# Optimization experiments

Hardware: AMD Instinct MI355X
Metric: run time of the kernel (lower is better)

Reference implementation:

```python
import jax, jax.numpy as jnp
import numpy as np

A = -0.75  # PyTorch bicubic coefficient (a=-0.75)


def _cubic_taps(n):
    # output coord i maps to src = i/2 - 0.25 (align_corners=False, scale=2)
    i = np.arange(2 * n)
    src = i / 2.0 - 0.25
    base = np.floor(src).astype(np.int64)
    t = src - base
    offs = np.array([-1, 0, 1, 2])
    idx = np.clip(base[:, None] + offs[None, :], 0, n - 1)  # (2n,4) replicate border
    d = np.abs(t[:, None] - offs[None, :])
    w = np.where(d <= 1.0,
                 (A + 2) * d ** 3 - (A + 3) * d ** 2 + 1.0,
                 A * d ** 3 - 5 * A * d ** 2 + 8 * A * d - 4 * A)
    return jnp.asarray(idx), jnp.asarray(w.astype(np.float32))


def _upsample2_bicubic(x):
    B, C, H, W = x.shape
    ih, wh = _cubic_taps(H)
    iw, ww = _cubic_taps(W)
    x = (x[:, :, ih, :] * wh[None, None, :, :, None]).sum(3)   # (B,C,2H,W)
    x = (x[:, :, :, iw] * ww[None, None, None, :, :]).sum(4)   # (B,C,2H,2W)
    return x


def _conv2d(x, w, b, pad):
    y = jax.lax.conv_general_dilated(x, w, (1, 1), ((pad, pad), (pad, pad)),
                                     dimension_numbers=('NCHW', 'OIHW', 'NCHW'))
    return y + b[None, :, None, None]


def _instance_norm(x, w, b, eps=1e-5):
    m = x.mean(axis=(2, 3), keepdims=True)
    v = x.var(axis=(2, 3), keepdims=True)
    return (x - m) * jax.lax.rsqrt(v + eps) * w[None, :, None, None] + b[None, :, None, None]


def _prelu(x, a):
    return jnp.where(x >= 0, x, a * x)


def _unfold5(x):
    # 5x5 neighborhoods, pad=2 -> (B, C, 25, H, W); row-major kernel tap order
    B, C, H, W = x.shape
    xp = jnp.pad(x, ((0, 0), (0, 0), (2, 2), (2, 2)))
    return jnp.stack([xp[:, :, i:i + H, j:j + W] for i in range(5) for j in range(5)], axis=2)


def _forward(input, feature, conv1_w, conv1_b, in1_w, in1_b, prelu1_a,
             conv2_w, conv2_b, in2_w, in2_b, prelu2_a,
             res_w, res_b, feat_w, feat_b, pac_w, pac_b):
    # main mapping: conv-IN-PReLU x2
    y = _prelu(_instance_norm(_conv2d(input, conv1_w, conv1_b, 1), in1_w, in1_b), prelu1_a)
    y = _prelu(_instance_norm(_conv2d(y, conv2_w, conv2_b, 1), in2_w, in2_b), prelu2_a)
    # residual 1x1 mapping (in_channels != out_channels)
    y = y + _conv2d(input, res_w, res_b, 0)
    y = _upsample2_bicubic(y)                               # (B,O,2H,2W)
    # PAC guidance: gaussian kernel from 1x1-mapped feature, normalized over window
    g = _conv2d(feature, feat_w, feat_b, 0)                 # (B,O,2H,2W)
    gcols = _unfold5(g)                                     # (B,O,25,2H,2W)
    diff2 = ((gcols - g[:, :, None]) ** 2).sum(axis=1)      # (B,25,2H,2W)
    kern = jnp.exp(-0.5 * diff2)
    kern = kern / kern.sum(axis=1, keepdims=True)           # normalize_kernel=True
    xcols = _unfold5(y)                                     # (B,O,25,2H,2W)
    O, Ci = pac_w.shape[0], pac_w.shape[1]
    out = jnp.einsum('ocp,bcphw,bphw->bohw', pac_w.reshape(O, Ci, 25), xcols, kern)
    return out + pac_b[None, :, None, None]


def setup_inputs() -> dict:
    key = jax.random.key(0)
    ks = jax.random.split(key, 8)
    Cin, Cout, Cf = 256, 128, 128
    B, H, W = 2, 48, 48
    f32 = jnp.float32

    def w(k, shape, fan_in):
        return jax.random.normal(k, shape, f32) / np.float32(np.sqrt(fan_in))

    return {
        'input': jax.random.normal(ks[0], (B, Cin, H, W), f32),
        'feature': jax.random.normal(ks[1], (B, Cf, 2 * H, 2 * W), f32),
        'conv1_w': w(ks[2], (Cout, Cin, 3, 3), Cin * 9), 'conv1_b': jnp.zeros((Cout,), f32),
        'in1_w': jnp.ones((Cout,), f32), 'in1_b': jnp.zeros((Cout,), f32),
        'prelu1_a': jnp.asarray(0.25, f32),
        'conv2_w': w(ks[3], (Cout, Cout, 3, 3), Cout * 9), 'conv2_b': jnp.zeros((Cout,), f32),
        'in2_w': jnp.ones((Cout,), f32), 'in2_b': jnp.zeros((Cout,), f32),
        'prelu2_a': jnp.asarray(0.25, f32),
        'res_w': w(ks[4], (Cout, Cin, 1, 1), Cin), 'res_b': jnp.zeros((Cout,), f32),
        'feat_w': w(ks[5], (Cout, Cf, 1, 1), Cf), 'feat_b': jnp.zeros((Cout,), f32),
        'pac_w': w(ks[6], (Cout, Cout, 5, 5), Cout * 25), 'pac_b': jnp.zeros((Cout,), f32),
    }


def reference(input, feature, conv1_w, conv1_b, in1_w, in1_b, prelu1_a,
              conv2_w, conv2_b, in2_w, in2_b, prelu2_a,
              res_w, res_b, feat_w, feat_b, pac_w, pac_b):
    return _forward(input, feature, conv1_w, conv1_b, in1_w, in1_b, prelu1_a,
                    conv2_w, conv2_b, in2_w, in2_b, prelu2_a,
                    res_w, res_b, feat_w, feat_b, pac_w, pac_b)
```

## Files before the change

kernel.cpp:

```cpp
#include <hip/hip_runtime.h>
#include <hip/hip_bf16.h>

typedef __attribute__((ext_vector_type(8))) short bf16x8;
typedef __attribute__((ext_vector_type(4))) float f32x4;

constexpr int B   = 2;
constexpr int CIN = 256;
constexpr int CO  = 128;
constexpr int H = 48, W = 48;
constexpr int H2 = 96, W2 = 96;
constexpr int NPIX1 = H * W;
constexpr int NPIX2 = H2 * W2;
constexpr int NS = 4;

__device__ inline ushort f2bf(float v)
{
  __hip_bfloat16 h = __float2bfloat16(v);
  return *reinterpret_cast<ushort*>(&h);
}

__global__ __launch_bounds__(256) void prep_weights_kernel(
    const float* __restrict__ pac_w, const float* __restrict__ conv1_w,
    const float* __restrict__ conv2_w, const float* __restrict__ feat_w,
    const float* __restrict__ res_w,
    ushort* __restrict__ wbb, ushort* __restrict__ wt1, ushort* __restrict__ wt2,
    ushort* __restrict__ fwb, ushort* __restrict__ wrb)
{
  int blk = blockIdx.x, tid = threadIdx.x;
  if (blk < 1600) {
    int idx = blk * 256 + tid;
    int c = idx & 127, o = (idx >> 7) & 127, p = idx >> 14;
    wbb[idx] = f2bf(pac_w[((size_t)o * CO + c) * 25 + p]);
  } else if (blk < 2752) {
    int idx = (blk - 1600) * 256 + tid;
    int ci = idx & 255, o = (idx >> 8) & 127, tap = idx >> 15;
    wt1[idx] = f2bf(conv1_w[((size_t)o * CIN + ci) * 9 + tap]);
  } else if (blk < 3328) {
    int idx = (blk - 2752) * 256 + tid;
    int ci = idx & 127, o = (idx >> 7) & 127, tap = idx >> 14;
    wt2[idx] = f2bf(conv2_w[((size_t)o * CO + ci) * 9 + tap]);
  } else if (blk < 3392) {
    int idx = (blk - 3328) * 256 + tid;
    fwb[idx] = f2bf(feat_w[idx]);
  } else {
    int idx = (blk - 3392) * 256 + tid;
    wrb[idx] = f2bf(res_w[idx]);
  }
}

__global__ __launch_bounds__(256) void cvt_both_kernel(
    const float* __restrict__ input, const float* __restrict__ feature,
    ushort* __restrict__ xinh, ushort* __restrict__ fh)
{
  __shared__ float lt[32][65];
  int tid = threadIdx.x;
  if (blockIdx.x < 576) {
    int blk = blockIdx.x;
    int cg = blk & 7;
    int pc = (blk >> 3) % 36;
    int b  = blk / (8 * 36);
    int c0 = cg * 32, pix0 = pc * 64;
#pragma unroll
    for (int r = 0; r < 8; r++) {
      int c_l = r * 4 + (tid >> 6), px = tid & 63;
      lt[c_l][px] = input[((size_t)b * CIN + c0 + c_l) * NPIX1 + pix0 + px];
    }
    __syncthreads();
    int c_l = tid & 31;
#pragma unroll
    for (int r = 0; r < 8; r++) {
      int px = r * 8 + (tid >> 5);
      xinh[((size_t)b * NPIX1 + pix0 + px) * CIN + c0 + c_l] = f2bf(lt[c_l][px]);
    }
  } else {
    int blk = blockIdx.x - 576;
    int cg = blk & 3;
    int pc = (blk >> 2) % 144;
    int b  = blk / (4 * 144);
    int c0 = cg * 32, pix0 = pc * 64;
#pragma unroll
    for (int r = 0; r < 8; r++) {
      int c_l = r * 4 + (tid >> 6), px = tid & 63;
      lt[c_l][px] = feature[((size_t)b * CO + c0 + c_l) * NPIX2 + pix0 + px];
    }
    __syncthreads();
    int c_l = tid & 31;
#pragma unroll
    for (int r = 0; r < 8; r++) {
      int px = r * 8 + (tid >> 5);
      fh[((size_t)b * NPIX2 + pix0 + px) * CO + c0 + c_l] = f2bf(lt[c_l][px]);
    }
  }
}

template<int CIg>
__device__ __forceinline__ void conv3_body(
    int blk, int tid, char* smraw,
    const ushort* __restrict__ xh, const ushort* __restrict__ wt,
    float* __restrict__ pout)
{
  constexpr int CS = CIg / NS;
  constexpr int G  = CS / 8;
  constexpr int KC = CS / 32;
  ushort* xt = (ushort*)smraw;
  int tile = blk % 36;
  int s = (blk / 36) & 3;
  int b = blk / 144;
  int th = tile / 3, tw = tile % 3;
  int h0 = th * 4, w0 = tw * 16;
  int lane = tid & 63, wv = tid >> 6;
  int l15 = lane & 15, l4 = (lane >> 4) & 3;

  for (int q = tid; q < 108 * G; q += 256) {
    int pixi = q / G, g = q & (G - 1);
    int rh = pixi / 18, rw = pixi - rh * 18;
    int hg = h0 - 1 + rh, wg = w0 - 1 + rw;
    uint4 v{0u, 0u, 0u, 0u};
    if (hg >= 0 && hg < H && wg >= 0 && wg < W)
      v = *(const uint4*)(xh + (size_t)(b * NPIX1 + hg * W + wg) * CIg + s * CS + g * 8);
    *(uint4*)(xt + pixi * CS + ((g ^ (pixi & (G - 1))) * 8)) = v;
  }
  __syncthreads();

  int wo = wv * 32;
  const ushort* wbase = wt + (size_t)(wo + l15) * CIg + s * CS + l4 * 8;

  f32x4 acc0[4], acc1[4];
#pragma unroll
  for (int nf = 0; nf < 4; nf++) {
    acc0[nf] = {0.f, 0.f, 0.f, 0.f};
    acc1[nf] = {0.f, 0.f, 0.f, 0.f};
  }

  bf16x8 aC0[KC], aC1[KC], aN0[KC], aN1[KC];
#pragma unroll
  for (int kc = 0; kc < KC; kc++) {
    aC0[kc] = *(const bf16x8*)(wbase + kc * 32);
    aC1[kc] = *(const bf16x8*)(wbase + 16 * CIg + kc * 32);
  }

#pragma unroll 1
  for (int tap = 0; tap < 9; ++tap) {
    if (tap < 8) {
      const ushort* wn = wbase + (size_t)(tap + 1) * 128 * CIg;
#pragma unroll
      for (int kc = 0; kc < KC; kc++) {
        aN0[kc] = *(const bf16x8*)(wn + kc * 32);
        aN1[kc] = *(const bf16x8*)(wn + 16 * CIg + kc * 32);
      }
    }
    int kh = (tap >= 6) ? 2 : ((tap >= 3) ? 1 : 0);
    int kw = tap - kh * 3;
#pragma unroll
    for (int kc = 0; kc < KC; kc++) {
#pragma unroll
      for (int nf = 0; nf < 4; nf++) {
        int pix = (nf + kh) * 18 + kw + l15;
        bf16x8 bb = *(const bf16x8*)(xt + pix * CS + (((kc * 4 + l4) ^ (pix & (G - 1))) * 8));
        acc0[nf] = __builtin_amdgcn_mfma_f32_16x16x32_bf16(aC0[kc], bb, acc0[nf], 0, 0, 0);
        acc1[nf] = __builtin_amdgcn_mfma_f32_16x16x32_bf16(aC1[kc], bb, acc1[nf], 0, 0, 0);
      }
    }
#pragma unroll
    for (int kc = 0; kc < KC; kc++) { aC0[kc] = aN0[kc]; aC1[kc] = aN1[kc]; }
  }

#pragma unroll
  for (int nf = 0; nf < 4; nf++) {
    int pixg = (h0 + nf) * W + w0 + l15;
#pragma unroll
    for (int r = 0; r < 4; r++) {
      int o = wo + l4 * 4 + r;
      pout[((size_t)(s * B + b) * CO + o) * NPIX1 + pixg] = acc0[nf][r];
      pout[((size_t)(s * B + b) * CO + o + 16) * NPIX1 + pixg] = acc1[nf][r];
    }
  }
}

__device__ __forceinline__ void gemm_res_body(
    int blk, int tid, char* smraw,
    const ushort* __restrict__ xh, const ushort* __restrict__ wrb,
    const float* __restrict__ bias, float* __restrict__ out)
{
  ushort* xt = (ushort*)smraw;
  int pc = blk % 72;
  int b  = blk / 72;
  int pix0 = pc * 32;
  int lane = tid & 63, wv = tid >> 6;
  int l15 = lane & 15, l4 = (lane >> 4) & 3;

  for (int q = tid; q < 1024; q += 256) {
    int pixi = q >> 5, g = q & 31;
    uint4 v = *(const uint4*)(xh + (((size_t)b * NPIX1 + pix0 + pixi) << 8) + (g << 3));
    *(uint4*)(xt + (pixi << 8) + ((g ^ (pixi & 31)) << 3)) = v;
  }
  __syncthreads();

  int wo = wv * 32;
  const ushort* wbase = wrb + (size_t)(wo + l15) * CIN + l4 * 8;
  bf16x8 a0[8], a1[8];
#pragma unroll
  for (int kc = 0; kc < 8; kc++) {
    a0[kc] = *(const bf16x8*)(wbase + kc * 32);
    a1[kc] = *(const bf16x8*)(wbase + 16 * CIN + kc * 32);
  }
  f32x4 acc0[2], acc1[2];
#pragma unroll
  for (int nf = 0; nf < 2; nf++) {
    acc0[nf] = {0.f, 0.f, 0.f, 0.f};
    acc1[nf] = {0.f, 0.f, 0.f, 0.f};
  }
#pragma unroll
  for (int nf = 0; nf < 2; nf++) {
    int pix = nf * 16 + l15;
    int base = pix << 8;
    int sw = pix & 31;
#pragma unroll
    for (int kc = 0; kc < 8; kc++) {
      bf16x8 bb = *(const bf16x8*)(xt + base + ((((kc << 2) + l4) ^ sw) << 3));
      acc0[nf] = __builtin_amdgcn_mfma_f32_16x16x32_bf16(a0[kc], bb, acc0[nf], 0, 0, 0);
      acc1[nf] = __builtin_amdgcn_mfma_f32_16x16x32_bf16(a1[kc], bb, acc1[nf], 0, 0, 0);
    }
  }
#pragma unroll
  for (int nf = 0; nf < 2; nf++) {
    int gp = pix0 + nf * 16 + l15;
#pragma unroll
    for (int r = 0; r < 4; r++) {
      int o = wo + l4 * 4 + r;
      out[((size_t)b * CO + o) * NPIX1 + gp] = acc0[nf][r] + bias[o];
      out[((size_t)b * CO + o + 16) * NPIX1 + gp] = acc1[nf][r] + bias[o + 16];
    }
  }
}

__device__ __forceinline__ void gemm1x1_body(
    int blk, int tid, char* smraw,
    const ushort* __restrict__ fh, const ushort* __restrict__ fwb,
    const float* __restrict__ bias, float* __restrict__ out)
{
  ushort* xt = (ushort*)smraw;
  int pc = blk % 144;
  int b  = blk / 144;
  int pix0 = pc * 64;
  int lane = tid & 63, wv = tid >> 6;
  int l15 = lane & 15, l4 = (lane >> 4) & 3;

  for (int q = tid; q < 1024; q += 256) {
    int pixi = q >> 4, g = q & 15;
    uint4 v = *(const uint4*)(fh + (((size_t)b * NPIX2 + pix0 + pixi) << 7) + (g << 3));
    *(uint4*)(xt + (pixi << 7) + ((g ^ (pixi & 15)) << 3)) = v;
  }
  __syncthreads();

  int wo = wv * 32;
  const ushort* wbase = fwb + (size_t)(wo + l15) * CO + l4 * 8;
  bf16x8 a0[4], a1[4];
#pragma unroll
  for (int kc = 0; kc < 4; kc++) {
    a0[kc] = *(const bf16x8*)(wbase + kc * 32);
    a1[kc] = *(const bf16x8*)(wbase + 16 * CO + kc * 32);
  }
  f32x4 acc0[4], acc1[4];
#pragma unroll
  for (int nf = 0; nf < 4; nf++) {
    acc0[nf] = {0.f, 0.f, 0.f, 0.f};
    acc1[nf] = {0.f, 0.f, 0.f, 0.f};
  }
#pragma unroll
  for (int nf = 0; nf < 4; nf++) {
    int pix = nf * 16 + l15;
    int base = pix << 7;
    int sw = pix & 15;
#pragma unroll
    for (int kc = 0; kc < 4; kc++) {
      bf16x8 bb = *(const bf16x8*)(xt + base + ((((kc << 2) + l4) ^ sw) << 3));
      acc0[nf] = __builtin_amdgcn_mfma_f32_16x16x32_bf16(a0[kc], bb, acc0[nf], 0, 0, 0);
      acc1[nf] = __builtin_amdgcn_mfma_f32_16x16x32_bf16(a1[kc], bb, acc1[nf], 0, 0, 0);
    }
  }
#pragma unroll
  for (int nf = 0; nf < 4; nf++) {
    int gp = pix0 + nf * 16 + l15;
#pragma unroll
    for (int r = 0; r < 4; r++) {
      int o = wo + l4 * 4 + r;
      out[((size_t)b * CO + o) * NPIX2 + gp] = acc0[nf][r] + bias[o];
      out[((size_t)b * CO + o + 16) * NPIX2 + gp] = acc1[nf][r] + bias[o + 16];
    }
  }
}

__global__ __launch_bounds__(256, 4) void mega1_kernel(
    const ushort* __restrict__ xinh, const ushort* __restrict__ wt1,
    float* __restrict__ pws,
    const ushort* __restrict__ wrb, const float* __restrict__ res_b,
    float* __restrict__ radd,
    const ushort* __restrict__ fh, const ushort* __restrict__ fwb,
    const float* __restrict__ feat_b, float* __restrict__ g)
{
  __shared__ __align__(16) char sm[16384];
  int blk = blockIdx.x, tid = threadIdx.x;
  if (blk < 288)      conv3_body<CIN>(blk, tid, sm, xinh, wt1, pws);
  else if (blk < 432) gemm_res_body(blk - 288, tid, sm, xinh, wrb, res_b, radd);
  else                gemm1x1_body(blk - 432, tid, sm, fh, fwb, feat_b, g);
}

__device__ __forceinline__ void kern_part_body(
    int blk, int tid, char* smraw,
    const float* __restrict__ g, float* __restrict__ pd2)
{
  float (*gt)[480] = (float(*)[480])smraw;
  int s = blk & 3;
  int tile = (blk >> 2) % 36;
  int b = blk / (4 * 36);
  int ty = tile / 6, tx = tile % 6;
  int h0 = ty * 16, w0 = tx * 16;
  int px = tid & 15, py = tid >> 4;
  float d2[25];
#pragma unroll
  for (int p = 0; p < 25; p++) d2[p] = 0.f;

  int cbase = s * 32;
#pragma unroll 1
  for (int cc = 0; cc < 32; cc += 8) {
    for (int idx = tid; idx < 3200; idx += 256) {
      int c_l = idx / 400, r = idx - c_l * 400;
      int rh = r / 20, rw = r - rh * 20;
      int hh = h0 - 2 + rh, ww = w0 - 2 + rw;
      float v = 0.f;
      if (hh >= 0 && hh < H2 && ww >= 0 && ww < W2)
        v = g[((size_t)b * CO + cbase + cc + c_l) * NPIX2 + hh * W2 + ww];
      gt[c_l][rh * 24 + rw] = v;
    }
    __syncthreads();
#pragma unroll
    for (int c_l = 0; c_l < 8; c_l++) {
      float ctr = gt[c_l][(py + 2) * 24 + px + 2];
#pragma unroll
      for (int dy = 0; dy < 5; dy++)
#pragma unroll
        for (int dx = 0; dx < 5; dx++) {
          float d = gt[c_l][(py + dy) * 24 + px + dx] - ctr;
          d2[dy * 5 + dx] += d * d;
        }
    }
    __syncthreads();
  }
  float* op = pd2 + ((size_t)((b * 36 + tile) * 4 + s) * 25) * 256 + tid;
#pragma unroll
  for (int p = 0; p < 25; p++) op[(size_t)p * 256] = d2[p];
}

__global__ __launch_bounds__(256, 4) void mega2_kernel(
    const ushort* __restrict__ t1h, const ushort* __restrict__ wt2,
    float* __restrict__ pws,
    const float* __restrict__ g, float* __restrict__ pd2)
{
  __shared__ __align__(16) char sm[15360];
  int blk = blockIdx.x, tid = threadIdx.x;
  if (blk < 288) conv3_body<CO>(blk, tid, sm, t1h, wt2, pws);
  else           kern_part_body(blk - 288, tid, sm, g, pd2);
}

__device__ __forceinline__ void reduce2_body(
    int bc, int tid,
    const float* __restrict__ pout, const float* __restrict__ cbias,
    const float* __restrict__ inw, const float* __restrict__ inb,
    const float* __restrict__ alpha_p, const float* __restrict__ radd,
    float* __restrict__ outf)
{
  int c = bc & 127;
  float bia = cbias[c];
  float v[9];
  float s = 0.f, s2 = 0.f;
#pragma unroll
  for (int i = 0; i < 9; i++) {
    size_t base = (size_t)bc * NPIX1 + tid + i * 256;
    float x = pout[base];
#pragma unroll
    for (int k = 1; k < NS; k++) x += pout[(size_t)k * B * CO * NPIX1 + base];
    x += bia;
    v[i] = x; s += x; s2 += x * x;
  }
#pragma unroll
  for (int off = 32; off > 0; off >>= 1) {
    s  += __shfl_down(s, off);
    s2 += __shfl_down(s2, off);
  }
  __shared__ float rs[4], rs2[4];
  int wid = tid >> 6, lane = tid & 63;
  if (lane == 0) { rs[wid] = s; rs2[wid] = s2; }
  __syncthreads();
  float S  = rs[0] + rs[1] + rs[2] + rs[3];
  float S2 = rs2[0] + rs2[1] + rs2[2] + rs2[3];
  float mean = S * (1.f / NPIX1);
  float var  = S2 * (1.f / NPIX1) - mean * mean;
  float inv  = rsqrtf(var + 1e-5f);
  float sc = inw[c] * inv;
  float sh = inb[c] - mean * sc;
  float a = *alpha_p;
#pragma unroll
  for (int i = 0; i < 9; i++) {
    size_t base = (size_t)bc * NPIX1 + tid + i * 256;
    float o = v[i] * sc + sh;
    o = (o >= 0.f) ? o : a * o;
    outf[base] = o + radd[base];
  }
}

__device__ __forceinline__ void kern_fin_body(
    int blk, int tid,
    const float* __restrict__ pd2, float* __restrict__ kern)
{
  int tile = blk % 36, b = blk / 36;
  int ty = tile / 6, tx = tile % 6;
  int h0 = ty * 16, w0 = tx * 16;
  int px = tid & 15, py = tid >> 4;
  const float* ip = pd2 + ((size_t)(b * 36 + tile) * 4 * 25) * 256 + tid;
  float e[25];
  float sum = 0.f;
#pragma unroll
  for (int p = 0; p < 25; p++) {
    float d = 0.f;
#pragma unroll
    for (int s = 0; s < 4; s++) d += ip[(size_t)(s * 25 + p) * 256];
    e[p] = __expf(-0.5f * d);
    sum += e[p];
  }
  float inv = 1.f / sum;
  int pixg = (h0 + py) * W2 + w0 + px;
  float* op = kern + ((size_t)b * NPIX2 + pixg) * 32;
#pragma unroll
  for (int p = 0; p < 25; p++) op[p] = e[p] * inv;
}

__global__ __launch_bounds__(256) void mega3_kernel(
    const float* __restrict__ pws, const float* __restrict__ conv2_b,
    const float* __restrict__ in2_w, const float* __restrict__ in2_b,
    const float* __restrict__ prelu2_a, const float* __restrict__ radd,
    float* __restrict__ t2,
    const float* __restrict__ pd2, float* __restrict__ kern)
{
  int blk = blockIdx.x, tid = threadIdx.x;
  if (blk < 256) reduce2_body(blk, tid, pws, conv2_b, in2_w, in2_b, prelu2_a, radd, t2);
  else           kern_fin_body(blk - 256, tid, pd2, kern);
}

__global__ __launch_bounds__(256) void reduce1_stats_kernel(
    const float* __restrict__ pout, const float* __restrict__ inw,
    const float* __restrict__ inb, float* __restrict__ scsh,
    float* __restrict__ outred)
{
  int bc = blockIdx.x, tid = threadIdx.x, c = bc & 127;
  float s = 0.f, s2 = 0.f;
#pragma unroll
  for (int i = 0; i < 9; i++) {
    size_t base = (size_t)bc * NPIX1 + tid + i * 256;
    float x = pout[base];
#pragma unroll
    for (int k = 1; k < NS; k++) x += pout[(size_t)k * B * CO * NPIX1 + base];
    outred[base] = x;
    s += x; s2 += x * x;
  }
#pragma unroll
  for (int off = 32; off > 0; off >>= 1) {
    s  += __shfl_down(s, off);
    s2 += __shfl_down(s2, off);
  }
  __shared__ float rs[4], rs2[4];
  int wid = tid >> 6, lane = tid & 63;
  if (lane == 0) { rs[wid] = s; rs2[wid] = s2; }
  __syncthreads();
  if (tid == 0) {
    float S  = rs[0] + rs[1] + rs[2] + rs[3];
    float S2 = rs2[0] + rs2[1] + rs2[2] + rs2[3];
    float mean = S * (1.f / NPIX1);
    float var  = S2 * (1.f / NPIX1) - mean * mean;
    float inv  = rsqrtf(var + 1e-5f);
    float sc = inw[c] * inv;
    scsh[2 * bc]     = sc;
    scsh[2 * bc + 1] = inb[c] - mean * sc;
  }
}

__global__ __launch_bounds__(256) void in_apply_hwc_kernel(
    const float* __restrict__ red, const float* __restrict__ scsh,
    const float* __restrict__ alpha_p, ushort* __restrict__ outh)
{
  int blk = blockIdx.x;
  int cg = blk & 3;
  int pc = (blk >> 2) % 36;
  int b  = blk / (4 * 36);
  int c0 = cg * 32, pix0 = pc * 64;
  int tid = threadIdx.x;
  float a = *alpha_p;
  __shared__ float lt[32][65];
#pragma unroll
  for (int r = 0; r < 8; r++) {
    int c_l = r * 4 + (tid >> 6), px = tid & 63;
    float x = red[((size_t)b * CO + c0 + c_l) * NPIX1 + pix0 + px];
    float sc = scsh[2 * (b * CO + c0 + c_l)];
    float sh = scsh[2 * (b * CO + c0 + c_l) + 1];
    float o = x * sc + sh;
    lt[c_l][px] = (o >= 0.f) ? o : a * o;
  }
  __syncthreads();
  int c_l = tid & 31;
#pragma unroll
  for (int r = 0; r < 8; r++) {
    int px = r * 8 + (tid >> 5);
    outh[((size_t)b * NPIX1 + pix0 + px) * CO + c0 + c_l] = f2bf(lt[c_l][px]);
  }
}

__device__ inline void bicubic_taps(int i, int n, int* r, float* w)
{
  const float we[4] = {-0.03515625f, 0.26171875f, 0.87890625f, -0.10546875f};
  bool odd = (i & 1);
  int base = (i >> 1) + (odd ? 0 : -1);
#pragma unroll
  for (int q = 0; q < 4; q++) {
    int rr = base + q - 1;
    r[q] = rr < 0 ? 0 : (rr > n - 1 ? n - 1 : rr);
    w[q] = odd ? we[3 - q] : we[q];
  }
}

__global__ __launch_bounds__(256) void upsample_t_kernel(
    const float* __restrict__ in, ushort* __restrict__ outh)
{
  int blk = blockIdx.x;
  int cg = blk & 3;
  int i  = (blk >> 2) % H2;
  int b  = blk / (4 * H2);
  int c0 = cg * 32;
  int tid = threadIdx.x;

  int rh[4]; float wh[4];
  bicubic_taps(i, H, rh, wh);

  __shared__ float ls[4 * 48 * 33];
  for (int k = 0; k < 24; k++) {
    int q = tid + k * 256;
    int ww = q % 48;
    int a  = (q / 48) & 3;
    int c_l = q / 192;
    ls[(a * 48 + ww) * 33 + c_l] =
        in[((size_t)b * CO + c0 + c_l) * NPIX1 + rh[a] * W + ww];
  }
  __syncthreads();

  int c_l = tid & 31;
#pragma unroll
  for (int rep = 0; rep < 12; rep++) {
    int j = rep * 8 + (tid >> 5);
    int rwj[4]; float wwj[4];
    bicubic_taps(j, W, rwj, wwj);
    float s = 0.f;
#pragma unroll
    for (int a = 0; a < 4; a++) {
      float r = 0.f;
#pragma unroll
      for (int q = 0; q < 4; q++)
        r += wwj[q] * ls[(a * 48 + rwj[q]) * 33 + c_l];
      s += wh[a] * r;
    }
    outh[((size_t)(b * H2 + i) * W2 + j) * CO + c0 + c_l] = f2bf(s);
  }
}

__global__ __launch_bounds__(256, 2) void pac_mfma_kernel(
    const ushort* __restrict__ xh,
    const float* __restrict__ kern,
    const ushort* __restrict__ wb,
    const float* __restrict__ bias, float* __restrict__ out)
{
  int blk = blockIdx.x;
  int og = blk & 1;
  int tw = (blk >> 1) % 6;
  int th = (blk >> 1) / 6 % 12;
  int b  = blk / (2 * 6 * 12);
  int h0 = th * 8, w0 = tw * 16;
  int tid = threadIdx.x, lane = tid & 63, wv = tid >> 6;
  int l15 = lane & 15, l4 = (lane >> 4) & 3;

  __shared__ ushort xt[240 * 128];
  __shared__ float kt[128][33];

  for (int q = tid; q < 3840; q += 256) {
    int pixi = q >> 4, cb = q & 15;
    int rh = pixi / 20, rw = pixi - rh * 20;
    int hg = h0 - 2 + rh, wg = w0 - 2 + rw;
    uint4 v{0u, 0u, 0u, 0u};
    if (hg >= 0 && hg < H2 && wg >= 0 && wg < W2)
      v = *(const uint4*)(xh + ((((size_t)b * H2 + hg) * W2 + wg) << 7) + (cb << 3));
    *(uint4*)(xt + (pixi << 7) + ((cb ^ (pixi & 15)) << 3)) = v;
  }
  for (int q = tid; q < 1024; q += 256) {
    int pixl = q >> 3, poff = (q & 7) << 2;
    int r = pixl >> 4, col = pixl & 15;
    const float* kp = kern + ((size_t)b * NPIX2 + (h0 + r) * W2 + w0 + col) * 32 + poff;
    float4 kv = *(const float4*)kp;
    kt[pixl][poff] = kv.x; kt[pixl][poff + 1] = kv.y;
    kt[pixl][poff + 2] = kv.z; kt[pixl][poff + 3] = kv.w;
  }
  __syncthreads();

  int wo = og * 64 + wv * 16;
  const ushort* wbase = wb + (size_t)(wo + l15) * CO + l4 * 8;

  f32x4 acc[8];
#pragma unroll
  for (int nf = 0; nf < 8; nf++) acc[nf] = {0.f, 0.f, 0.f, 0.f};

  bf16x8 aC[4], aN[4];
#pragma unroll
  for (int kc = 0; kc < 4; kc++)
    aC[kc] = *(const bf16x8*)(wbase + kc * 32);

  int dy = 0, dx = 0;
#pragma unroll 1
  for (int p = 0; p < 25; ++p) {
    if (p < 24) {
      const ushort* wnext = wbase + (size_t)(p + 1) * CO * CO;
#pragma unroll
      for (int kc = 0; kc < 4; kc++)
        aN[kc] = *(const bf16x8*)(wnext + kc * 32);
    }
#pragma unroll
    for (int nf = 0; nf < 8; nf++) {
      int pix = (nf + dy) * 20 + dx + l15;
      int base = pix << 7;
      int sw = pix & 15;
      f32x4 y = {0.f, 0.f, 0.f, 0.f};
#pragma unroll
      for (int kc = 0; kc < 4; kc++) {
        bf16x8 bb = *(const bf16x8*)(xt + base + (((kc * 4 + l4) ^ sw) << 3));
        y = __builtin_amdgcn_mfma_f32_16x16x32_bf16(aC[kc], bb, y, 0, 0, 0);
      }
      float ks = kt[(nf << 4) + l15][p];
#pragma unroll
      for (int r = 0; r < 4; r++) acc[nf][r] += ks * y[r];
    }
#pragma unroll
    for (int kc = 0; kc < 4; kc++) aC[kc] = aN[kc];
    if (++dx == 5) { dx = 0; dy++; }
  }

#pragma unroll
  for (int nf = 0; nf < 8; nf++) {
    int gpix = (h0 + nf) * W2 + w0 + l15;
#pragma unroll
    for (int r = 0; r < 4; r++) {
      int o = wo + l4 * 4 + r;
      out[((size_t)b * CO + o) * NPIX2 + gpix] = acc[nf][r] + bias[o];
    }
  }
}

extern "C" void kernel_launch(void* const* d_in, const int* in_sizes, int n_in,
                              void* d_out, int out_size, void* d_ws, size_t ws_size,
                              hipStream_t stream)
{
  (void)in_sizes; (void)n_in; (void)out_size; (void)ws_size;
  const float* input    = (const float*)d_in[0];
  const float* feature  = (const float*)d_in[1];
  const float* conv1_w  = (const float*)d_in[2];
  const float* conv1_b  = (const float*)d_in[3];
  const float* in1_w    = (const float*)d_in[4];
  const float* in1_b    = (const float*)d_in[5];
  const float* prelu1_a = (const float*)d_in[6];
  const float* conv2_w  = (const float*)d_in[7];
  const float* conv2_b  = (const float*)d_in[8];
  const float* in2_w    = (const float*)d_in[9];
  const float* in2_b    = (const float*)d_in[10];
  const float* prelu2_a = (const float*)d_in[11];
  const float* res_w    = (const float*)d_in[12];
  const float* res_b    = (const float*)d_in[13];
  const float* feat_w   = (const float*)d_in[14];
  const float* feat_b   = (const float*)d_in[15];
  const float* pac_w    = (const float*)d_in[16];
  const float* pac_b    = (const float*)d_in[17];
  float* out = (float*)d_out;

  float* ws = (float*)d_ws;
  float*  kern = ws;
  ushort* t1h  = (ushort*)ws;
  ushort* wt2  = (ushort*)(ws + 294912);
  ushort* wt1  = (ushort*)(ws + 368640);
  float*  t2   = ws + 589824;
  float*  pws  = ws + 1179648;
  float*  g    = ws + 3538944;
  ushort* xinh = (ushort*)g;
  ushort* yh   = (ushort*)(ws + 5898240);
  ushort* wbb  = (ushort*)(ws + 7077888);
  float*  scsh = ws + 7282688;
  ushort* fh   = (ushort*)(ws + 7283200);
  ushort* fwb  = (ushort*)(ws + 8462848);
  ushort* wrb  = (ushort*)(ws + 8471040);
  float*  radd = ws + 8487424;
  float*  pd2  = ws + 9077248;
  ushort* xinh2 = (ushort*)(ws + 10920448);

  prep_weights_kernel<<<3520, 256, 0, stream>>>(
      pac_w, conv1_w, conv2_w, feat_w, res_w, wbb, wt1, wt2, fwb, wrb);
  cvt_both_kernel<<<1728, 256, 0, stream>>>(input, feature, xinh2, fh);

  mega1_kernel<<<720, 256, 0, stream>>>(
      xinh2, wt1, pws, wrb, res_b, radd, fh, fwb, feat_b, g);
  reduce1_stats_kernel<<<B * CO, 256, 0, stream>>>(pws, in1_w, in1_b, scsh, t2);
  in_apply_hwc_kernel<<<B * 36 * 4, 256, 0, stream>>>(t2, scsh, prelu1_a, t1h);
  mega2_kernel<<<576, 256, 0, stream>>>(t1h, wt2, pws, g, pd2);
  mega3_kernel<<<328, 256, 0, stream>>>(
      pws, conv2_b, in2_w, in2_b, prelu2_a, radd, t2, pd2, kern);
  upsample_t_kernel<<<B * H2 * 4, 256, 0, stream>>>(t2, yh);
  pac_mfma_kernel<<<B * 12 * 6 * 2, 256, 0, stream>>>(yh, kern, wbb, pac_b, out);
}
```

Before: 123.9 us.

## Split conv3 output channels across blocks and regroup kernel stages for co-scheduling

The 3x3 conv body now gives each block half the output channels (each wave 16 instead of 32), doubling the block count for conv1 and conv2 so more CUs have work. The weight prep and input/feature layout conversions are merged into one launch. The stage grouping is reshuffled: the distance-kernel partial runs alongside the IN1 stats reduce, and its finalize runs alongside IN1 apply. conv2 and reduce2 become standalone launches, and the kern buffer moves to its own workspace region. The cost is that each conv block reloads the same input tile for half the channels, and the IN2 reduce no longer overlaps other work.

```diff
diff --git a/kernel.cpp b/kernel.cpp
--- a/kernel.cpp
+++ b/kernel.cpp
@@ -19,13 +19,16 @@
   return *reinterpret_cast<ushort*>(&h);
 }
 
-__global__ __launch_bounds__(256) void prep_weights_kernel(
+__global__ __launch_bounds__(256) void prep_all_kernel(
     const float* __restrict__ pac_w, const float* __restrict__ conv1_w,
     const float* __restrict__ conv2_w, const float* __restrict__ feat_w,
-    const float* __restrict__ res_w,
+    const float* __restrict__ res_w, const float* __restrict__ input,
+    const float* __restrict__ feature,
     ushort* __restrict__ wbb, ushort* __restrict__ wt1, ushort* __restrict__ wt2,
-    ushort* __restrict__ fwb, ushort* __restrict__ wrb)
-{
+    ushort* __restrict__ fwb, ushort* __restrict__ wrb,
+    ushort* __restrict__ xinh, ushort* __restrict__ fh)
+{
+  __shared__ float lt[32][65];
   int blk = blockIdx.x, tid = threadIdx.x;
   if (blk < 1600) {
     int idx = blk * 256 + tid;
@@ -42,23 +45,14 @@
   } else if (blk < 3392) {
     int idx = (blk - 3328) * 256 + tid;
     fwb[idx] = f2bf(feat_w[idx]);
-  } else {
+  } else if (blk < 3520) {
     int idx = (blk - 3392) * 256 + tid;
     wrb[idx] = f2bf(res_w[idx]);
-  }
-}
-
-__global__ __launch_bounds__(256) void cvt_both_kernel(
-    const float* __restrict__ input, const float* __restrict__ feature,
-    ushort* __restrict__ xinh, ushort* __restrict__ fh)
-{
-  __shared__ float lt[32][65];
-  int tid = threadIdx.x;
-  if (blockIdx.x < 576) {
-    int blk = blockIdx.x;
-    int cg = blk & 7;
-    int pc = (blk >> 3) % 36;
-    int b  = blk / (8 * 36);
+  } else if (blk < 4096) {
+    int b2 = blk - 3520;
+    int cg = b2 & 7;
+    int pc = (b2 >> 3) % 36;
+    int b  = b2 / (8 * 36);
     int c0 = cg * 32, pix0 = pc * 64;
 #pragma unroll
     for (int r = 0; r < 8; r++) {
@@ -73,10 +67,10 @@
       xinh[((size_t)b * NPIX1 + pix0 + px) * CIN + c0 + c_l] = f2bf(lt[c_l][px]);
     }
   } else {
-    int blk = blockIdx.x - 576;
-    int cg = blk & 3;
-    int pc = (blk >> 2) % 144;
-    int b  = blk / (4 * 144);
+    int b2 = blk - 4096;
+    int cg = b2 & 3;
+    int pc = (b2 >> 2) % 144;
+    int b  = b2 / (4 * 144);
     int c0 = cg * 32, pix0 = pc * 64;
 #pragma unroll
     for (int r = 0; r < 8; r++) {
@@ -105,7 +99,8 @@
   ushort* xt = (ushort*)smraw;
   int tile = blk % 36;
   int s = (blk / 36) & 3;
-  int b = blk / 144;
+  int oh = (blk / 144) & 1;
+  int b = blk / 288;
   int th = tile / 3, tw = tile % 3;
   int h0 = th * 4, w0 = tw * 16;
   int lane = tid & 63, wv = tid >> 6;
@@ -122,32 +117,25 @@
   }
   __syncthreads();
 
-  int wo = wv * 32;
+  int wo = oh * 64 + wv * 16;
   const ushort* wbase = wt + (size_t)(wo + l15) * CIg + s * CS + l4 * 8;
 
-  f32x4 acc0[4], acc1[4];
-#pragma unroll
-  for (int nf = 0; nf < 4; nf++) {
-    acc0[nf] = {0.f, 0.f, 0.f, 0.f};
-    acc1[nf] = {0.f, 0.f, 0.f, 0.f};
-  }
-
-  bf16x8 aC0[KC], aC1[KC], aN0[KC], aN1[KC];
-#pragma unroll
-  for (int kc = 0; kc < KC; kc++) {
-    aC0[kc] = *(const bf16x8*)(wbase + kc * 32);
-    aC1[kc] = *(const bf16x8*)(wbase + 16 * CIg + kc * 32);
-  }
+  f32x4 acc[4];
+#pragma unroll
+  for (int nf = 0; nf < 4; nf++) acc[nf] = {0.f, 0.f, 0.f, 0.f};
+
+  bf16x8 aC[KC], aN[KC];
+#pragma unroll
+  for (int kc = 0; kc < KC; kc++)
+    aC[kc] = *(const bf16x8*)(wbase + kc * 32);
 
 #pragma unroll 1
   for (int tap = 0; tap < 9; ++tap) {
     if (tap < 8) {
       const ushort* wn = wbase + (size_t)(tap + 1) * 128 * CIg;
 #pragma unroll
-      for (int kc = 0; kc < KC; kc++) {
-        aN0[kc] = *(const bf16x8*)(wn + kc * 32);
-        aN1[kc] = *(const bf16x8*)(wn + 16 * CIg + kc * 32);
-      }
+      for (int kc = 0; kc < KC; kc++)
+        aN[kc] = *(const bf16x8*)(wn + kc * 32);
     }
     int kh = (tap >= 6) ? 2 : ((tap >= 3) ? 1 : 0);
     int kw = tap - kh * 3;
@@ -157,12 +145,11 @@
       for (int nf = 0; nf < 4; nf++) {
         int pix = (nf + kh) * 18 + kw + l15;
         bf16x8 bb = *(const bf16x8*)(xt + pix * CS + (((kc * 4 + l4) ^ (pix & (G - 1))) * 8));
-        acc0[nf] = __builtin_amdgcn_mfma_f32_16x16x32_bf16(aC0[kc], bb, acc0[nf], 0, 0, 0);
-        acc1[nf] = __builtin_amdgcn_mfma_f32_16x16x32_bf16(aC1[kc], bb, acc1[nf], 0, 0, 0);
+        acc[nf] = __builtin_amdgcn_mfma_f32_16x16x32_bf16(aC[kc], bb, acc[nf], 0, 0, 0);
       }
     }
 #pragma unroll
-    for (int kc = 0; kc < KC; kc++) { aC0[kc] = aN0[kc]; aC1[kc] = aN1[kc]; }
+    for (int kc = 0; kc < KC; kc++) aC[kc] = aN[kc];
   }
 
 #pragma unroll
@@ -171,8 +158,7 @@
 #pragma unroll
     for (int r = 0; r < 4; r++) {
       int o = wo + l4 * 4 + r;
-      pout[((size_t)(s * B + b) * CO + o) * NPIX1 + pixg] = acc0[nf][r];
-      pout[((size_t)(s * B + b) * CO + o + 16) * NPIX1 + pixg] = acc1[nf][r];
+      pout[((size_t)(s * B + b) * CO + o) * NPIX1 + pixg] = acc[nf][r];
     }
   }
 }
@@ -291,7 +277,7 @@
   }
 }
 
-__global__ __launch_bounds__(256, 4) void mega1_kernel(
+__global__ __launch_bounds__(256, 4) void megaA_kernel(
     const ushort* __restrict__ xinh, const ushort* __restrict__ wt1,
     float* __restrict__ pws,
     const ushort* __restrict__ wrb, const float* __restrict__ res_b,
@@ -301,158 +287,18 @@
 {
   __shared__ __align__(16) char sm[16384];
   int blk = blockIdx.x, tid = threadIdx.x;
-  if (blk < 288)      conv3_body<CIN>(blk, tid, sm, xinh, wt1, pws);
-  else if (blk < 432) gemm_res_body(blk - 288, tid, sm, xinh, wrb, res_b, radd);
-  else                gemm1x1_body(blk - 432, tid, sm, fh, fwb, feat_b, g);
-}
-
-__device__ __forceinline__ void kern_part_body(
-    int blk, int tid, char* smraw,
-    const float* __restrict__ g, float* __restrict__ pd2)
-{
-  float (*gt)[480] = (float(*)[480])smraw;
-  int s = blk & 3;
-  int tile = (blk >> 2) % 36;
-  int b = blk / (4 * 36);
-  int ty = tile / 6, tx = tile % 6;
-  int h0 = ty * 16, w0 = tx * 16;
-  int px = tid & 15, py = tid >> 4;
-  float d2[25];
-#pragma unroll
-  for (int p = 0; p < 25; p++) d2[p] = 0.f;
-
-  int cbase = s * 32;
-#pragma unroll 1
-  for (int cc = 0; cc < 32; cc += 8) {
-    for (int idx = tid; idx < 3200; idx += 256) {
-      int c_l = idx / 400, r = idx - c_l * 400;
-      int rh = r / 20, rw = r - rh * 20;
-      int hh = h0 - 2 + rh, ww = w0 - 2 + rw;
-      float v = 0.f;
-      if (hh >= 0 && hh < H2 && ww >= 0 && ww < W2)
-        v = g[((size_t)b * CO + cbase + cc + c_l) * NPIX2 + hh * W2 + ww];
-      gt[c_l][rh * 24 + rw] = v;
-    }
-    __syncthreads();
-#pragma unroll
-    for (int c_l = 0; c_l < 8; c_l++) {
-      float ctr = gt[c_l][(py + 2) * 24 + px + 2];
-#pragma unroll
-      for (int dy = 0; dy < 5; dy++)
-#pragma unroll
-        for (int dx = 0; dx < 5; dx++) {
-          float d = gt[c_l][(py + dy) * 24 + px + dx] - ctr;
-          d2[dy * 5 + dx] += d * d;
-        }
-    }
-    __syncthreads();
-  }
-  float* op = pd2 + ((size_t)((b * 36 + tile) * 4 + s) * 25) * 256 + tid;
-#pragma unroll
-  for (int p = 0; p < 25; p++) op[(size_t)p * 256] = d2[p];
-}
-
-__global__ __launch_bounds__(256, 4) void mega2_kernel(
-    const ushort* __restrict__ t1h, const ushort* __restrict__ wt2,
-    float* __restrict__ pws,
-    const float* __restrict__ g, float* __restrict__ pd2)
-{
-  __shared__ __align__(16) char sm[15360];
-  int blk = blockIdx.x, tid = threadIdx.x;
-  if (blk < 288) conv3_body<CO>(blk, tid, sm, t1h, wt2, pws);
-  else           kern_part_body(blk - 288, tid, sm, g, pd2);
-}
-
-__device__ __forceinline__ void reduce2_body(
+  if (blk < 576)      conv3_body<CIN>(blk, tid, sm, xinh, wt1, pws);
+  else if (blk < 720) gemm_res_body(blk - 576, tid, sm, xinh, wrb, res_b, radd);
+  else                gemm1x1_body(blk - 720, tid, sm, fh, fwb, feat_b, g);
+}
+
+__device__ __forceinline__ void reduce1_body(
     int bc, int tid,
-    const float* __restrict__ pout, const float* __restrict__ cbias,
-    const float* __restrict__ inw, const float* __restrict__ inb,
-    const float* __restrict__ alpha_p, const float* __restrict__ radd,
-    float* __restrict__ outf)
-{
-  int c = bc & 127;
-  float bia = cbias[c];
-  float v[9];
-  float s = 0.f, s2 = 0.f;
-#pragma unroll
-  for (int i = 0; i < 9; i++) {
-    size_t base = (size_t)bc * NPIX1 + tid + i * 256;
-    float x = pout[base];
-#pragma unroll
-    for (int k = 1; k < NS; k++) x += pout[(size_t)k * B * CO * NPIX1 + base];
-    x += bia;
-    v[i] = x; s += x; s2 += x * x;
-  }
-#pragma unroll
-  for (int off = 32; off > 0; off >>= 1) {
-    s  += __shfl_down(s, off);
-    s2 += __shfl_down(s2, off);
-  }
-  __shared__ float rs[4], rs2[4];
-  int wid = tid >> 6, lane = tid & 63;
-  if (lane == 0) { rs[wid] = s; rs2[wid] = s2; }
-  __syncthreads();
-  float S  = rs[0] + rs[1] + rs[2] + rs[3];
-  float S2 = rs2[0] + rs2[1] + rs2[2] + rs2[3];
-  float mean = S * (1.f / NPIX1);
-  float var  = S2 * (1.f / NPIX1) - mean * mean;
-  float inv  = rsqrtf(var + 1e-5f);
-  float sc = inw[c] * inv;
-  float sh = inb[c] - mean * sc;
-  float a = *alpha_p;
-#pragma unroll
-  for (int i = 0; i < 9; i++) {
-    size_t base = (size_t)bc * NPIX1 + tid + i * 256;
-    float o = v[i] * sc + sh;
-    o = (o >= 0.f) ? o : a * o;
-    outf[base] = o + radd[base];
-  }
-}
-
-__device__ __forceinline__ void kern_fin_body(
-    int blk, int tid,
-    const float* __restrict__ pd2, float* __restrict__ kern)
-{
-  int tile = blk % 36, b = blk / 36;
-  int ty = tile / 6, tx = tile % 6;
-  int h0 = ty * 16, w0 = tx * 16;
-  int px = tid & 15, py = tid >> 4;
-  const float* ip = pd2 + ((size_t)(b * 36 + tile) * 4 * 25) * 256 + tid;
-  float e[25];
-  float sum = 0.f;
-#pragma unroll
-  for (int p = 0; p < 25; p++) {
-    float d = 0.f;
-#pragma unroll
-    for (int s = 0; s < 4; s++) d += ip[(size_t)(s * 25 + p) * 256];
-    e[p] = __expf(-0.5f * d);
-    sum += e[p];
-  }
-  float inv = 1.f / sum;
-  int pixg = (h0 + py) * W2 + w0 + px;
-  float* op = kern + ((size_t)b * NPIX2 + pixg) * 32;
-#pragma unroll
-  for (int p = 0; p < 25; p++) op[p] = e[p] * inv;
-}
-
-__global__ __launch_bounds__(256) void mega3_kernel(
-    const float* __restrict__ pws, const float* __restrict__ conv2_b,
-    const float* __restrict__ in2_w, const float* __restrict__ in2_b,
-    const float* __restrict__ prelu2_a, const float* __restrict__ radd,
-    float* __restrict__ t2,
-    const float* __restrict__ pd2, float* __restrict__ kern)
-{
-  int blk = blockIdx.x, tid = threadIdx.x;
-  if (blk < 256) reduce2_body(blk, tid, pws, conv2_b, in2_w, in2_b, prelu2_a, radd, t2);
-  else           kern_fin_body(blk - 256, tid, pd2, kern);
-}
-
-__global__ __launch_bounds__(256) void reduce1_stats_kernel(
     const float* __restrict__ pout, const float* __restrict__ inw,
     const float* __restrict__ inb, float* __restrict__ scsh,
     float* __restrict__ outred)
 {
-  int bc = blockIdx.x, tid = threadIdx.x, c = bc & 127;
+  int c = bc & 127;
   float s = 0.f, s2 = 0.f;
 #pragma unroll
   for (int i = 0; i < 9; i++) {
@@ -484,16 +330,73 @@
   }
 }
 
-__global__ __launch_bounds__(256) void in_apply_hwc_kernel(
+__device__ __forceinline__ void kern_part_body(
+    int blk, int tid, char* smraw,
+    const float* __restrict__ g, float* __restrict__ pd2)
+{
+  float (*gt)[480] = (float(*)[480])smraw;
+  int s = blk & 3;
+  int tile = (blk >> 2) % 36;
+  int b = blk / (4 * 36);
+  int ty = tile / 6, tx = tile % 6;
+  int h0 = ty * 16, w0 = tx * 16;
+  int px = tid & 15, py = tid >> 4;
+  float d2[25];
+#pragma unroll
+  for (int p = 0; p < 25; p++) d2[p] = 0.f;
+
+  int cbase = s * 32;
+#pragma unroll 1
+  for (int cc = 0; cc < 32; cc += 8) {
+    for (int idx = tid; idx < 3200; idx += 256) {
+      int c_l = idx / 400, r = idx - c_l * 400;
+      int rh = r / 20, rw = r - rh * 20;
+      int hh = h0 - 2 + rh, ww = w0 - 2 + rw;
+      float v = 0.f;
+      if (hh >= 0 && hh < H2 && ww >= 0 && ww < W2)
+        v = g[((size_t)b * CO + cbase + cc + c_l) * NPIX2 + hh * W2 + ww];
+      gt[c_l][rh * 24 + rw] = v;
+    }
+    __syncthreads();
+#pragma unroll
+    for (int c_l = 0; c_l < 8; c_l++) {
+      float ctr = gt[c_l][(py + 2) * 24 + px + 2];
+#pragma unroll
+      for (int dy = 0; dy < 5; dy++)
+#pragma unroll
+        for (int dx = 0; dx < 5; dx++) {
+          float d = gt[c_l][(py + dy) * 24 + px + dx] - ctr;
+          d2[dy * 5 + dx] += d * d;
+        }
+    }
+    __syncthreads();
+  }
+  float* op = pd2 + ((size_t)((b * 36 + tile) * 4 + s) * 25) * 256 + tid;
+#pragma unroll
+  for (int p = 0; p < 25; p++) op[(size_t)p * 256] = d2[p];
+}
+
+__global__ __launch_bounds__(256, 4) void megaB_kernel(
+    const float* __restrict__ pws, const float* __restrict__ in1_w,
+    const float* __restrict__ in1_b, float* __restrict__ scsh,
+    float* __restrict__ t2red,
+    const float* __restrict__ g, float* __restrict__ pd2)
+{
+  __shared__ __align__(16) char sm[15360];
+  int blk = blockIdx.x, tid = threadIdx.x;
+  if (blk < 256) reduce1_body(blk, tid, pws, in1_w, in1_b, scsh, t2red);
+  else           kern_part_body(blk - 256, tid, sm, g, pd2);
+}
+
+__device__ __forceinline__ void apply1_body(
+    int blk, int tid,
     const float* __restrict__ red, const float* __restrict__ scsh,
     const float* __restrict__ alpha_p, ushort* __restrict__ outh)
 {
-  int blk = blockIdx.x;
   int cg = blk & 3;
   int pc = (blk >> 2) % 36;
   int b  = blk / (4 * 36);
   int c0 = cg * 32, pix0 = pc * 64;
-  int tid = threadIdx.x;
   float a = *alpha_p;
   __shared__ float lt[32][65];
 #pragma unroll
@@ -511,6 +414,95 @@
   for (int r = 0; r < 8; r++) {
     int px = r * 8 + (tid >> 5);
     outh[((size_t)b * NPIX1 + pix0 + px) * CO + c0 + c_l] = f2bf(lt[c_l][px]);
+  }
+}
+
+__device__ __forceinline__ void kern_fin_body(
+    int blk, int tid,
+    const float* __restrict__ pd2, float* __restrict__ kern)
+{
+  int tile = blk % 36, b = blk / 36;
+  int ty = tile / 6, tx = tile % 6;
+  int h0 = ty * 16, w0 = tx * 16;
+  int px = tid & 15, py = tid >> 4;
+  const float* ip = pd2 + ((size_t)(b * 36 + tile) * 4 * 25) * 256 + tid;
+  float e[25];
+  float sum = 0.f;
+#pragma unroll
+  for (int p = 0; p < 25; p++) {
+    float d = 0.f;
+#pragma unroll
+    for (int s = 0; s < 4; s++) d += ip[(size_t)(s * 25 + p) * 256];
+    e[p] = __expf(-0.5f * d);
+    sum += e[p];
+  }
+  float inv = 1.f / sum;
+  int pixg = (h0 + py) * W2 + w0 + px;
+  float* op = kern + ((size_t)b * NPIX2 + pixg) * 32;
+#pragma unroll
+  for (int p = 0; p < 25; p++) op[p] = e[p] * inv;
+}
+
+__global__ __launch_bounds__(256) void megaC_kernel(
+    const float* __restrict__ t2red, const float* __restrict__ scsh,
+    const float* __restrict__ prelu1_a, ushort* __restrict__ t1h,
+    const float* __restrict__ pd2, float* __restrict__ kern)
+{
+  int blk = blockIdx.x, tid = threadIdx.x;
+  if (blk < 288) apply1_body(blk, tid, t2red, scsh, prelu1_a, t1h);
+  else           kern_fin_body(blk - 288, tid, pd2, kern);
+}
+
+__global__ __launch_bounds__(256, 4) void conv2_kernel(
+    const ushort* __restrict__ t1h, const ushort* __restrict__ wt2,
+    float* __restrict__ pws)
+{
+  __shared__ __align__(16) char sm[6912];
+  conv3_body<CO>(blockIdx.x, threadIdx.x, sm, t1h, wt2, pws);
+}
+
+__global__ __launch_bounds__(256) void reduce2_kernel(
+    const float* __restrict__ pout, const float* __restrict__ cbias,
+    const float* __restrict__ inw, const float* __restrict__ inb,
+    const float* __restrict__ alpha_p, const float* __restrict__ radd,
+    float* __restrict__ outf)
+{
+  int bc = blockIdx.x, tid = threadIdx.x, c = bc & 127;
+  float bia = cbias[c];
+  float v[9];
+  float s = 0.f, s2 = 0.f;
+#pragma unroll
+  for (int i = 0; i < 9; i++) {
+    size_t base = (size_t)bc * NPIX1 + tid + i * 256;
+    float x = pout[base];
+#pragma unroll
+    for (int k = 1; k < NS; k++) x += pout[(size_t)k * B * CO * NPIX1 + base];
+    x += bia;
+    v[i] = x; s += x; s2 += x * x;
+  }
+#pragma unroll
+  for (int off = 32; off > 0; off >>= 1) {
+    s  += __shfl_down(s, off);
+    s2 += __shfl_down(s2, off);
+  }
+  __shared__ float rs[4], rs2[4];
+  int wid = tid >> 6, lane = tid & 63;
+  if (lane == 0) { rs[wid] = s; rs2[wid] = s2; }
+  __syncthreads();
+  float S  = rs[0] + rs[1] + rs[2] + rs[3];
+  float S2 = rs2[0] + rs2[1] + rs2[2] + rs2[3];
+  float mean = S * (1.f / NPIX1);
+  float var  = S2 * (1.f / NPIX1) - mean * mean;
+  float inv  = rsqrtf(var + 1e-5f);
+  float sc = inw[c] * inv;
+  float sh = inb[c] - mean * sc;
+  float a = *alpha_p;
+#pragma unroll
+  for (int i = 0; i < 9; i++) {
+    size_t base = (size_t)bc * NPIX1 + tid + i * 256;
+    float o = v[i] * sc + sh;
+    o = (o >= 0.f) ? o : a * o;
+    outf[base] = o + radd[base];
   }
 }
 
@@ -685,14 +677,12 @@
   float* out = (float*)d_out;
 
   float* ws = (float*)d_ws;
-  float*  kern = ws;
   ushort* t1h  = (ushort*)ws;
   ushort* wt2  = (ushort*)(ws + 294912);
   ushort* wt1  = (ushort*)(ws + 368640);
   float*  t2   = ws + 589824;
   float*  pws  = ws + 1179648;
   float*  g    = ws + 3538944;
-  ushort* xinh = (ushort*)g;
   ushort* yh   = (ushort*)(ws + 5898240);
   ushort* wbb  = (ushort*)(ws + 7077888);
   float*  scsh = ws + 7282688;
@@ -701,19 +691,19 @@
   ushort* wrb  = (ushort*)(ws + 8471040);
   float*  radd = ws + 8487424;
   float*  pd2  = ws + 9077248;
-  ushort* xinh2 = (ushort*)(ws + 10920448);
-
-  prep_weights_kernel<<<3520, 256, 0, stream>>>(
-      pac_w, conv1_w, conv2_w, feat_w, res_w, wbb, wt1, wt2, fwb, wrb);
-  cvt_both_kernel<<<1728, 256, 0, stream>>>(input, feature, xinh2, fh);
-
-  mega1_kernel<<<720, 256, 0, stream>>>(
-      xinh2, wt1, pws, wrb, res_b, radd, fh, fwb, feat_b, g);
-  reduce1_stats_kernel<<<B * CO, 256, 0, stream>>>(pws, in1_w, in1_b, scsh, t2);
-  in_apply_hwc_kernel<<<B * 36 * 4, 256, 0, stream>>>(t2, scsh, prelu1_a, t1h);
-  mega2_kernel<<<576, 256, 0, stream>>>(t1h, wt2, pws, g, pd2);
-  mega3_kernel<<<328, 256, 0, stream>>>(
-      pws, conv2_b, in2_w, in2_b, prelu2_a, radd, t2, pd2, kern);
+  ushort* xinh = (ushort*)(ws + 10920448);
+  float*  kern = ws + 11215360;
+
+  prep_all_kernel<<<5248, 256, 0, stream>>>(
+      pac_w, conv1_w, conv2_w, feat_w, res_w, input, feature,
+      wbb, wt1, wt2, fwb, wrb, xinh, fh);
+  megaA_kernel<<<1008, 256, 0, stream>>>(
+      xinh, wt1, pws, wrb, res_b, radd, fh, fwb, feat_b, g);
+  megaB_kernel<<<544, 256, 0, stream>>>(pws, in1_w, in1_b, scsh, t2, g, pd2);
+  megaC_kernel<<<360, 256, 0, stream>>>(t2, scsh, prelu1_a, t1h, pd2, kern);
+  conv2_kernel<<<576, 256, 0, stream>>>(t1h, wt2, pws);
+  reduce2_kernel<<<B * CO, 256, 0, stream>>>(
+      pws, conv2_b, in2_w, in2_b, prelu2_a, radd, t2);
   upsample_t_kernel<<<B * H2 * 4, 256, 0, stream>>>(t2, yh);
   pac_mfma_kernel<<<B * 12 * 6 * 2, 256, 0, stream>>>(yh, kern, wbb, pac_b, out);
 }
```

Measured after the change: 121.5 us (median of 2 runs). Within noise of the previous version (-1.9%).
